# Kernel tuning notes

Hardware: AMD Instinct MI355X
Metric: run time of the kernel (lower is better)

## Reference

```python
import jax, jax.numpy as jnp
import numpy as np

D_MODEL = 1024
N_HEADS = 16
D_HEAD = 64


def setup_inputs() -> dict:
    key = jax.random.key(0)
    ks = jax.random.split(key, 9)
    B, T = 2, 2048
    s_in = 1.0 / np.sqrt(D_MODEL)
    s_o = 1.0 / np.sqrt(N_HEADS * D_HEAD)
    return {
        "x": jax.random.normal(ks[0], (B, T, D_MODEL), dtype=jnp.float32),
        "wq": jax.random.normal(ks[1], (D_MODEL, N_HEADS * D_HEAD), dtype=jnp.float32) * s_in,
        "bq": jax.random.normal(ks[2], (N_HEADS * D_HEAD,), dtype=jnp.float32) * 0.01,
        "wk": jax.random.normal(ks[3], (D_MODEL, N_HEADS * D_HEAD), dtype=jnp.float32) * s_in,
        "bk": jax.random.normal(ks[4], (N_HEADS * D_HEAD,), dtype=jnp.float32) * 0.01,
        "wv": jax.random.normal(ks[5], (D_MODEL, N_HEADS * D_HEAD), dtype=jnp.float32) * s_in,
        "bv": jax.random.normal(ks[6], (N_HEADS * D_HEAD,), dtype=jnp.float32) * 0.01,
        "wo": jax.random.normal(ks[7], (N_HEADS * D_HEAD, D_MODEL), dtype=jnp.float32) * s_o,
        "bo": jax.random.normal(ks[8], (D_MODEL,), dtype=jnp.float32) * 0.01,
    }


def reference(x, wq, bq, wk, bk, wv, bv, wo, bo):
    B, T, _ = x.shape
    H, Dh = N_HEADS, D_HEAD
    # projections -> [B, H, T, Dh]
    q = (x @ wq + bq).reshape(B, T, H, Dh).transpose(0, 2, 1, 3)
    k = (x @ wk + bk).reshape(B, T, H, Dh).transpose(0, 2, 1, 3)
    v = (x @ wv + bv).reshape(B, T, H, Dh).transpose(0, 2, 1, 3)
    scale = 1.0 / np.sqrt(Dh).astype(np.float32)
    attn = jnp.einsum("bhqd,bhkd->bhqk", q, k) * scale  # [B,H,T,T]
    causal = jnp.tril(jnp.ones((T, T), dtype=bool))
    attn = jnp.where(causal, attn, jnp.float32(-jnp.inf))
    attn = jax.nn.softmax(attn, axis=-1)
    out = jnp.einsum("bhqk,bhkd->bhqd", attn, v)  # [B,H,T,Dh]
    out = out.transpose(0, 2, 1, 3).reshape(B, T, H * Dh)
    return out @ wo + bo
```

## Files before the change

kernel.cpp:

```cpp
#include <hip/hip_runtime.h>
#include <math.h>

#define D_MODEL 1024
#define N_HEADS 16
#define D_HEAD  64
#define B_SZ    2
#define T_SEQ   2048
#define WN_ELEMS (1024u * 1024u)

typedef short bf16x8 __attribute__((ext_vector_type(8)));
typedef short bf16x4 __attribute__((ext_vector_type(4)));
typedef float f32x4  __attribute__((ext_vector_type(4)));
typedef unsigned short us4 __attribute__((ext_vector_type(4)));

__device__ __forceinline__ unsigned short f2bf(float f) {
  union { float f; unsigned u; } v; v.f = f;
  unsigned r = v.u + 0x7FFFu + ((v.u >> 16) & 1u);
  return (unsigned short)(r >> 16);
}
__device__ __forceinline__ float bf2f(unsigned short s) {
  union { unsigned u; float f; } v; v.u = ((unsigned)s) << 16;
  return v.f;
}
__device__ __forceinline__ unsigned pack2_rtz(float lo, float hi) {
  union { float f; unsigned u; } a, b; a.f = hi; b.f = lo;
  return __builtin_amdgcn_perm(a.u, b.u, 0x07060302u);
}

__device__ __forceinline__ void async_copy16(const unsigned short* g, unsigned short* l) {
  __builtin_amdgcn_global_load_lds(
      (__attribute__((address_space(1))) void*)(g),
      (__attribute__((address_space(3))) void*)(l), 16, 0, 0);
}


__device__ __forceinline__ unsigned short* opart_ptr(
    unsigned short* wtd, unsigned short* xbd, int p) {
  const size_t off = (size_t)p * 2048;
  const size_t RA  = (size_t)3 * 1024 * 1024;
  return (off < RA) ? (wtd + off) : (xbd + (off - RA));
}

__global__ __launch_bounds__(256) void conv_all(
    const float* __restrict__ x,
    const float* __restrict__ wq, const float* __restrict__ wk,
    const float* __restrict__ wv, const float* __restrict__ wo,
    unsigned short* __restrict__ wt, unsigned short* __restrict__ xb)
{
  const int z = blockIdx.z;
  if (z < 4) {
    const float* W = (z == 0) ? wq : (z == 1) ? wk : (z == 2) ? wv : wo;
    unsigned short* O = wt + (size_t)z * WN_ELEMS;
    __shared__ float t[32][33];
    const int tx = threadIdx.x & 31, ty = threadIdx.x >> 5;
    const int kb = blockIdx.x * 32, nb = blockIdx.y * 32;
    #pragma unroll
    for (int i = 0; i < 4; i++)
      t[ty + i * 8][tx] = W[(size_t)(kb + ty + i * 8) * D_MODEL + nb + tx];
    __syncthreads();
    const int tid = threadIdx.x;
    const int mi  = tid >> 7;
    const int f   = (tid & 127) * 4;
    const int qd  = f >> 7;
    const int lrr = (f >> 3) & 15;
    const int e0  = f & 7;
    const int kt  = kb >> 6, hf = (kb >> 5) & 1, fbn = nb >> 5;
    us4 o;
    #pragma unroll
    for (int j = 0; j < 4; j++)
      o[j] = f2bf(t[qd * 8 + e0 + j][mi * 16 + lrr]);
    *(us4*)&O[((size_t)(fbn * 16 + kt) * 4 + (mi * 2 + hf)) * 512 + f] = o;
  } else {
    const int row = (z - 4) * 1024 + blockIdx.y * 32 + (threadIdx.x >> 3);
    const int col = blockIdx.x * 32 + (threadIdx.x & 7) * 4;
    float4 v = *(const float4*)&x[(size_t)row * D_MODEL + col];
    us4 o = { f2bf(v.x), f2bf(v.y), f2bf(v.z), f2bf(v.w) };
    *(us4*)&xb[(size_t)row * D_MODEL + col] = o;
  }
}

#define BKg 64
#define NTg (D_MODEL / BKg)
#define QSCALE 0.180336879f

__global__ __launch_bounds__(256) void qkv_gemm(
    const unsigned short* __restrict__ A, const unsigned short* __restrict__ Bt,
    const float* __restrict__ bq, const float* __restrict__ bk,
    const float* __restrict__ bv, unsigned short* __restrict__ qkv,
    unsigned short* __restrict__ vT)
{
  __shared__ unsigned short As[2][128 * BKg];

  const int tid  = threadIdx.x;
  const int wv   = tid >> 6;
  const int lane = tid & 63;
  const int lr   = lane & 15;
  const int quad = lane >> 4;
  const int wm   = wv >> 1;
  const int wn   = wv & 1;
  const int row0 = blockIdx.x * 128;
  const int col0 = blockIdx.y * 64;
  const int K = D_MODEL;

  const int mid = col0 >> 10;
  const float* bias = (mid == 0) ? bq : (mid == 1) ? bk : bv;

  f32x4 acc[8];
  #pragma unroll
  for (int i = 0; i < 8; i++) acc[i] = (f32x4){0.f, 0.f, 0.f, 0.f};

  auto stageA = [&](int buf, int k0) {
    #pragma unroll
    for (int it = 0; it < 4; it++) {
      const int gg = wv * 256 + it * 64 + lane;
      const int r  = gg >> 3;
      const int gc = ((gg & 7) ^ (r & 7)) * 8;
      async_copy16(A + (size_t)(row0 + r) * K + k0 + gc,
                   &As[buf][(size_t)(wv * 256 + it * 64) * 8]);
    }
  };

  const int wsel = (mid == 2) ? wn : wm;
  const int fb   = ((col0 & 1023) >> 5) + wsel;
  const unsigned short* Wp =
      Bt + (size_t)mid * WN_ELEMS + (size_t)fb * (16 * 2048) + lane * 8;

  auto loadW = [&](int kt, bf16x8 (&W)[2][2]) {
    #pragma unroll
    for (int mi = 0; mi < 2; mi++)
      #pragma unroll
      for (int hf = 0; hf < 2; hf++)
        W[mi][hf] = *(const bf16x8*)&Wp[((size_t)kt * 4 + mi * 2 + hf) * 512];
  };

  const int xrow = (mid == 2) ? wm : wn;

  bf16x8 Wc[2][2], Wn[2][2];
  loadW(0, Wc);
  stageA(0, 0);
  int cur = 0;

  auto kstep = [&](int t, bf16x8 (&Wuse)[2][2], bf16x8 (&Wpre)[2][2]) {
    __syncthreads();

    bf16x8 xF[4][2];
    #pragma unroll
    for (int hf = 0; hf < 2; hf++) {
      const int kc = ((hf * 4 + quad) ^ (lr & 7)) * 8;
      #pragma unroll
      for (int ni = 0; ni < 4; ni++)
        xF[ni][hf] = *(const bf16x8*)&As[cur][(xrow * 64 + ni * 16 + lr) * BKg + kc];
    }

    if (t + 1 < NTg) {
      stageA(cur ^ 1, (t + 1) * BKg);
      loadW(t + 1, Wpre);
    }

    if (mid == 2) {
      #pragma unroll
      for (int hf = 0; hf < 2; hf++)
        #pragma unroll
        for (int mi = 0; mi < 4; mi++)
          #pragma unroll
          for (int ni = 0; ni < 2; ni++)
            acc[mi * 2 + ni] = __builtin_amdgcn_mfma_f32_16x16x32_bf16(
                xF[mi][hf], Wuse[ni][hf], acc[mi * 2 + ni], 0, 0, 0);
    } else {
      #pragma unroll
      for (int hf = 0; hf < 2; hf++)
        #pragma unroll
        for (int mi = 0; mi < 2; mi++)
          #pragma unroll
          for (int ni = 0; ni < 4; ni++)
            acc[mi * 4 + ni] = __builtin_amdgcn_mfma_f32_16x16x32_bf16(
                Wuse[mi][hf], xF[ni][hf], acc[mi * 4 + ni], 0, 0, 0);
    }
    cur ^= 1;
  };

  #pragma unroll 1
  for (int t = 0; t < NTg; t += 2) {
    kstep(t,     Wc, Wn);
    kstep(t + 1, Wn, Wc);
  }

  if (mid == 2) {
    #pragma unroll
    for (int ni = 0; ni < 2; ni++) {
      const int nn = (col0 & 1023) + wn * 32 + ni * 16 + lr;
      const float bv_ = bias[nn];
      const int h = nn >> 6, d = nn & 63;
      #pragma unroll
      for (int mi = 0; mi < 4; mi++) {
        const int t0_ = row0 + wm * 64 + mi * 16 + quad * 4;
        const int b = t0_ >> 11, tl = t0_ & 2047;
        us4 o;
        #pragma unroll
        for (int i = 0; i < 4; i++) o[i] = f2bf(acc[mi * 2 + ni][i] + bv_);
        *(us4*)&vT[((size_t)(b * N_HEADS + h) * D_HEAD + d) * T_SEQ + tl] = o;
      }
    }
  } else {
    unsigned short* dst = qkv + (size_t)mid * (4096u * 1024u);
    const float qs = (mid == 0) ? QSCALE : 1.0f;
    #pragma unroll
    for (int ni = 0; ni < 4; ni++) {
      const int t = row0 + wn * 64 + ni * 16 + lr;
      const int b = t >> 11, tl = t & 2047;
      #pragma unroll
      for (int mi = 0; mi < 2; mi++) {
        const int f = (col0 & 1023) + wm * 32 + mi * 16 + quad * 4;
        const int h = f >> 6, d = f & 63;
        const float4 b4 = *(const float4*)&bias[f];
        us4 o;
        o[0] = f2bf((acc[mi * 4 + ni][0] + b4.x) * qs);
        o[1] = f2bf((acc[mi * 4 + ni][1] + b4.y) * qs);
        o[2] = f2bf((acc[mi * 4 + ni][2] + b4.z) * qs);
        o[3] = f2bf((acc[mi * 4 + ni][3] + b4.w) * qs);
        *(us4*)&dst[((size_t)(b * N_HEADS + h) * T_SEQ + tl) * D_HEAD + d] = o;
      }
    }
  }
}

__global__ __launch_bounds__(256) void mfma_gemm(
    const unsigned short* __restrict__ A, const unsigned short* __restrict__ Bt,
    const float* __restrict__ bias, float* __restrict__ C,
    int M, int N, int K)
{
  __shared__ unsigned short As[2][128 * BKg];

  const int tid  = threadIdx.x;
  const int wv   = tid >> 6;
  const int lane = tid & 63;
  const int lr   = lane & 15;
  const int quad = lane >> 4;
  const int wm   = wv >> 1;
  const int wn   = wv & 1;
  const int row0 = blockIdx.x * 128;
  const int col0 = blockIdx.y * 64;

  f32x4 acc[4][2];
  #pragma unroll
  for (int mi = 0; mi < 4; mi++)
    #pragma unroll
    for (int ni = 0; ni < 2; ni++) acc[mi][ni] = (f32x4){0.f, 0.f, 0.f, 0.f};

  auto stageA = [&](int buf, int k0) {
    #pragma unroll
    for (int it = 0; it < 4; it++) {
      const int gg = wv * 256 + it * 64 + lane;
      const int r  = gg >> 3;
      const int gc = ((gg & 7) ^ (r & 7)) * 8;
      async_copy16(A + (size_t)(row0 + r) * K + k0 + gc,
                   &As[buf][(size_t)(wv * 256 + it * 64) * 8]);
    }
  };

  const int fb = (col0 >> 5) + wn;
  const unsigned short* Wp = Bt + (size_t)fb * (16 * 2048) + lane * 8;
  auto loadW = [&](int kt, bf16x8 (&W)[2][2]) {
    #pragma unroll
    for (int ni = 0; ni < 2; ni++)
      #pragma unroll
      for (int hf = 0; hf < 2; hf++)
        W[ni][hf] = *(const bf16x8*)&Wp[((size_t)kt * 4 + ni * 2 + hf) * 512];
  };

  const int NT = K / BKg;
  bf16x8 Wc[2][2], Wn[2][2];
  loadW(0, Wc);
  stageA(0, 0);
  int cur = 0;

  auto kstep = [&](int t, bf16x8 (&Wuse)[2][2], bf16x8 (&Wpre)[2][2]) {
    __syncthreads();

    bf16x8 aF[4][2];
    #pragma unroll
    for (int hf = 0; hf < 2; hf++) {
      const int kc = ((hf * 4 + quad) ^ (lr & 7)) * 8;
      #pragma unroll
      for (int mi = 0; mi < 4; mi++)
        aF[mi][hf] = *(const bf16x8*)&As[cur][(wm * 64 + mi * 16 + lr) * BKg + kc];
    }

    if (t + 1 < NT) {
      stageA(cur ^ 1, (t + 1) * BKg);
      loadW(t + 1, Wpre);
    }

    #pragma unroll
    for (int hf = 0; hf < 2; hf++)
      #pragma unroll
      for (int mi = 0; mi < 4; mi++)
        #pragma unroll
        for (int ni = 0; ni < 2; ni++)
          acc[mi][ni] = __builtin_amdgcn_mfma_f32_16x16x32_bf16(
              aF[mi][hf], Wuse[ni][hf], acc[mi][ni], 0, 0, 0);
    cur ^= 1;
  };

  #pragma unroll 1
  for (int t = 0; t < NT; t += 2) {
    kstep(t,     Wc, Wn);
    kstep(t + 1, Wn, Wc);
  }

  #pragma unroll
  for (int ni = 0; ni < 2; ni++) {
    const int n = col0 + wn * 32 + ni * 16 + lr;
    const float bv = bias[n];
    #pragma unroll
    for (int mi = 0; mi < 4; mi++) {
      #pragma unroll
      for (int i = 0; i < 4; i++) {
        const int m = row0 + wm * 64 + mi * 16 + quad * 4 + i;
        C[(size_t)m * N + n] = acc[mi][ni][i] + bv;
      }
    }
  }
}

__global__ __launch_bounds__(256) void flash_part(
    const unsigned short* __restrict__ Q, const unsigned short* __restrict__ K,
    const unsigned short* __restrict__ Vt, unsigned short* __restrict__ Out,
    unsigned short* __restrict__ OpA, unsigned short* __restrict__ OpB,
    float* __restrict__ Lpart)
{
  const int bh = blockIdx.x;
  const int y  = blockIdx.y;
  int g, md;
  if (y < 28) { g = 15 - (y >> 1); md = 1 + (y & 1); }
  else        { g = 29 - y; md = 0; }

  const int b  = bh >> 4;
  const int h  = bh & 15;

  const unsigned short* Qb = Q  + (size_t)bh * T_SEQ * D_HEAD;
  const unsigned short* Kb = K  + (size_t)bh * T_SEQ * D_HEAD;
  const unsigned short* Vb = Vt + (size_t)bh * D_HEAD * T_SEQ;

  __shared__ __align__(16) unsigned short Ks[2][64 * 64];
  __shared__ __align__(16) unsigned short Vs[2][64 * 64];

  const int tid  = threadIdx.x;
  const int wv4  = tid >> 6;
  const int lane = tid & 63;
  const int lr   = lane & 15;
  const int quad = lane >> 4;

  const int qg      = 4 * g + wv4;
  const int q0      = qg * 32;
  const int my_full = 2 * g + 1 + (wv4 >> 1);
  const int tstart  = (md == 2) ? (g + 1) : 0;
  const int bend    = (md == 1) ? (g + 1) : (2 * g + 2);
  const int my_end  = (md == 1) ? (g + 1) : my_full;

  const int cbase = (tid & ~63);
  const int rr = tid >> 3;
  const int gcf = ((tid & 7) ^ (rr & 7)) * 8;
  const unsigned short* kp0 = Kb + (size_t)rr * D_HEAD + gcf;
  const unsigned short* vp0 = Vb + (size_t)rr * T_SEQ + gcf;

  auto stage = [&](int buf, int tile) {
    const unsigned short* kt = kp0 + (size_t)tile * (64 * D_HEAD);
    const unsigned short* vt = vp0 + (size_t)tile * 64;
    async_copy16(kt,                    &Ks[buf][(size_t)cbase * 8]);
    async_copy16(kt + 32 * D_HEAD,      &Ks[buf][(size_t)(256 + cbase) * 8]);
    async_copy16(vt,                    &Vs[buf][(size_t)cbase * 8]);
    async_copy16(vt + (size_t)32 * T_SEQ, &Vs[buf][(size_t)(256 + cbase) * 8]);
  };

  bf16x8 bQ[2][2];
  #pragma unroll
  for (int qb = 0; qb < 2; qb++)
    #pragma unroll
    for (int kh = 0; kh < 2; kh++)
      bQ[qb][kh] = *(const bf16x8*)&Qb[(size_t)(q0 + qb * 16 + lr) * D_HEAD + kh * 32 + quad * 8];

  f32x4 oacc[2][4];
  #pragma unroll
  for (int qb = 0; qb < 2; qb++)
    #pragma unroll
    for (int dt = 0; dt < 4; dt++) oacc[qb][dt] = (f32x4){0.f, 0.f, 0.f, 0.f};
  f32x4 lacc[2] = {(f32x4){0.f, 0.f, 0.f, 0.f}, (f32x4){0.f, 0.f, 0.f, 0.f}};

  const bf16x4 vONE = {(short)0x3F80, (short)0x3F80, (short)0x3F80, (short)0x3F80};

  int cur = 0;
  stage(0, tstart);

  for (int j = tstart; j < bend; j++) {
    __syncthreads();
    const bool act = (j < my_end);
    const unsigned short* KsB = &Ks[cur][0];
    const unsigned short* VsB = &Vs[cur][0];
    const int kv0 = j * 64;

    bf16x8 aK[4][2];
    bf16x4 aV[4][4];
    if (act) {
      #pragma unroll
      for (int nt = 0; nt < 4; nt++) {
        const int row = nt * 16 + lr;
        #pragma unroll
        for (int kh = 0; kh < 2; kh++) {
          const int sc = (kh * 4 + quad) ^ (row & 7);
          aK[nt][kh] = *(const bf16x8*)&KsB[row * 64 + sc * 8];
        }
      }
      #pragma unroll
      for (int dt = 0; dt < 4; dt++) {
        const int row = dt * 16 + lr;
        #pragma unroll
        for (int ks = 0; ks < 4; ks++) {
          const int sc = (ks * 2 + (quad >> 1)) ^ (row & 7);
          aV[dt][ks] = *(const bf16x4*)&VsB[row * 64 + sc * 8 + (quad & 1) * 4];
        }
      }
    }

    if (j + 1 < bend) stage(cur ^ 1, j + 1);

    if (act) {
      f32x4 sacc[2][4];
      __builtin_amdgcn_s_setprio(1);
      #pragma unroll
      for (int nt = 0; nt < 4; nt++) {
        #pragma unroll
        for (int qb = 0; qb < 2; qb++) {
          f32x4 c = (f32x4){0.f, 0.f, 0.f, 0.f};
          c = __builtin_amdgcn_mfma_f32_16x16x32_bf16(aK[nt][0], bQ[qb][0], c, 0, 0, 0);
          c = __builtin_amdgcn_mfma_f32_16x16x32_bf16(aK[nt][1], bQ[qb][1], c, 0, 0, 0);
          sacc[qb][nt] = c;
        }
      }
      __builtin_amdgcn_s_setprio(0);

      const bool diag = (j == my_full - 1);
      bf16x4 bP[2][4];
      #pragma unroll
      for (int qb = 0; qb < 2; qb++) {
        if (diag) {
          const int qcol = q0 + qb * 16 + lr;
          #pragma unroll
          for (int nt = 0; nt < 4; nt++)
            #pragma unroll
            for (int i = 0; i < 4; i++)
              if (kv0 + nt * 16 + quad * 4 + i > qcol) sacc[qb][nt][i] = -INFINITY;
        }
        #pragma unroll
        for (int nt = 0; nt < 4; nt++) {
          float p[4];
          #pragma unroll
          for (int i = 0; i < 4; i++)
            p[i] = __builtin_amdgcn_exp2f(sacc[qb][nt][i]);
          union { unsigned u[2]; bf16x4 v; } pk;
          pk.u[0] = pack2_rtz(p[0], p[1]);
          pk.u[1] = pack2_rtz(p[2], p[3]);
          bP[qb][nt] = pk.v;
        }
      }

      __builtin_amdgcn_s_setprio(1);
      #pragma unroll
      for (int ks = 0; ks < 4; ks++) {
        #pragma unroll
        for (int qb = 0; qb < 2; qb++) {
          lacc[qb] = __builtin_amdgcn_mfma_f32_16x16x16bf16_1k(
              vONE, bP[qb][ks], lacc[qb], 0, 0, 0);
          #pragma unroll
          for (int dt = 0; dt < 4; dt++)
            oacc[qb][dt] = __builtin_amdgcn_mfma_f32_16x16x16bf16_1k(
                aV[dt][ks], bP[qb][ks], oacc[qb][dt], 0, 0, 0);
        }
      }
      __builtin_amdgcn_s_setprio(0);
    }
    cur ^= 1;
  }

  float l_i[2] = {lacc[0][0], lacc[1][0]};

  if (md == 0) {
    #pragma unroll
    for (int qb = 0; qb < 2; qb++) {
      const float invl = __builtin_amdgcn_rcpf(l_i[qb]);
      const size_t orow = (size_t)(b * T_SEQ + q0 + qb * 16 + lr) * D_MODEL + h * D_HEAD;
      #pragma unroll
      for (int dt = 0; dt < 4; dt++) {
        us4 o;
        #pragma unroll
        for (int i = 0; i < 4; i++) o[i] = f2bf(oacc[qb][dt][i] * invl);
        *(us4*)&Out[orow + dt * 16 + quad * 4] = o;
      }
    }
  } else {
    const int s = md - 1;
    const int p = (bh * 56 + (qg - 8)) * 2 + s;
    unsigned short* Op = opart_ptr(OpA, OpB, p);
    if (quad == 0) {
      Lpart[(p * 2 + 0) * 16 + lr] = l_i[0];
      Lpart[(p * 2 + 1) * 16 + lr] = l_i[1];
    }
    #pragma unroll
    for (int qb = 0; qb < 2; qb++) {
      #pragma unroll
      for (int dt = 0; dt < 4; dt++) {
        us4 o;
        #pragma unroll
        for (int i = 0; i < 4; i++) o[i] = f2bf(oacc[qb][dt][i]);
        *(us4*)&Op[(size_t)(((qb * 4 + dt) * 64) + lane) * 4] = o;
      }
    }
  }
}

__global__ __launch_bounds__(64) void flash_reduce(
    unsigned short* __restrict__ OpA, unsigned short* __restrict__ OpB,
    const float* __restrict__ Lpart, unsigned short* __restrict__ Out)
{
  const int bh  = blockIdx.x;
  const int qgr = blockIdx.y;
  const int q0  = (8 + qgr) * 32;
  const int b   = bh >> 4;
  const int h   = bh & 15;
  const int lane = threadIdx.x;
  const int lr   = lane & 15;
  const int quad = lane >> 4;

  const int item = bh * 56 + qgr;
  const int p0 = item * 2, p1 = item * 2 + 1;
  const unsigned short* O0 = opart_ptr(OpA, OpB, p0);
  const unsigned short* O1 = opart_ptr(OpA, OpB, p1);

  #pragma unroll
  for (int qb = 0; qb < 2; qb++) {
    const float l0 = Lpart[(p0 * 2 + qb) * 16 + lr];
    const float l1 = Lpart[(p1 * 2 + qb) * 16 + lr];
    const float invL = __builtin_amdgcn_rcpf(l0 + l1);
    const size_t orow = (size_t)(b * T_SEQ + q0 + qb * 16 + lr) * D_MODEL + h * D_HEAD;
    #pragma unroll
    for (int dt = 0; dt < 4; dt++) {
      us4 o0 = *(const us4*)&O0[(size_t)(((qb * 4 + dt) * 64) + lane) * 4];
      us4 o1 = *(const us4*)&O1[(size_t)(((qb * 4 + dt) * 64) + lane) * 4];
      us4 o;
      #pragma unroll
      for (int i = 0; i < 4; i++)
        o[i] = f2bf((bf2f(o0[i]) + bf2f(o1[i])) * invL);
      *(us4*)&Out[orow + dt * 16 + quad * 4] = o;
    }
  }
}

extern "C" void kernel_launch(void* const* d_in, const int* in_sizes, int n_in,
                              void* d_out, int out_size, void* d_ws, size_t ws_size,
                              hipStream_t stream) {
  (void)in_sizes; (void)n_in; (void)out_size; (void)ws_size;

  const float* x  = (const float*)d_in[0];
  const float* wq = (const float*)d_in[1];
  const float* bq = (const float*)d_in[2];
  const float* wk = (const float*)d_in[3];
  const float* bk = (const float*)d_in[4];
  const float* wv = (const float*)d_in[5];
  const float* bv = (const float*)d_in[6];
  const float* wo = (const float*)d_in[7];
  const float* bo = (const float*)d_in[8];
  float* out = (float*)d_out;

  const int M = B_SZ * T_SEQ;
  const int N = D_MODEL;
  const int K = D_MODEL;
  const size_t MN = (size_t)M * N;
  const size_t WN = (size_t)N * N;

  unsigned short* wt    = (unsigned short*)d_ws;
  unsigned short* xb    = wt + 4 * WN;
  unsigned short* qkv   = xb + MN;
  unsigned short* qb    = qkv;
  unsigned short* kb    = qkv + MN;
  unsigned short* vT    = qkv + 2 * MN;
  unsigned short* attnb = vT + MN;
  float* Lpart = (float*)(attnb + MN);

  conv_all<<<dim3(32, 32, 8), dim3(256), 0, stream>>>(x, wq, wk, wv, wo, wt, xb);

  qkv_gemm<<<dim3(M / 128, 48), dim3(256), 0, stream>>>(xb, wt, bq, bk, bv, qkv, vT);

  flash_part<<<dim3(B_SZ * N_HEADS, 30), dim3(256), 0, stream>>>(
      qb, kb, vT, attnb, wt, xb, Lpart);
  flash_reduce<<<dim3(B_SZ * N_HEADS, 56), dim3(64), 0, stream>>>(
      wt, xb, Lpart, attnb);

  mfma_gemm<<<dim3(M / 128, N / 64), dim3(256), 0, stream>>>(attnb, wt + 3 * WN, bo, out, M, N, K);
}
```

Baseline: 184.7 us.

## Triple-buffer QKV GEMM loads with prefetch distance two and explicit vmcnt waits

Converts the QKV projection GEMM from double to triple buffering. Both the A tile in LDS and the W fragments in registers are now prefetched two k-steps ahead, and the loop is fully unrolled. Explicit s_waitcnt vmcnt plus an s_barrier replace the plain __syncthreads, so loads stay in flight across iterations. This is meant to hide global-memory latency better, at the cost of 50% more LDS and extra W registers, which may reduce occupancy.

```diff
diff --git a/kernel.cpp b/kernel.cpp
--- a/kernel.cpp
+++ b/kernel.cpp
@@ -89,7 +89,7 @@
     const float* __restrict__ bv, unsigned short* __restrict__ qkv,
     unsigned short* __restrict__ vT)
 {
-  __shared__ unsigned short As[2][128 * BKg];
+  __shared__ unsigned short As[3][128 * BKg];
 
   const int tid  = threadIdx.x;
   const int wv   = tid >> 6;
@@ -125,23 +125,28 @@
   const unsigned short* Wp =
       Bt + (size_t)mid * WN_ELEMS + (size_t)fb * (16 * 2048) + lane * 8;
 
-  auto loadW = [&](int kt, bf16x8 (&W)[2][2]) {
+  bf16x8 Wb[3][2][2];
+  auto loadW = [&](int kt, int bank) {
     #pragma unroll
     for (int mi = 0; mi < 2; mi++)
       #pragma unroll
       for (int hf = 0; hf < 2; hf++)
-        W[mi][hf] = *(const bf16x8*)&Wp[((size_t)kt * 4 + mi * 2 + hf) * 512];
+        Wb[bank][mi][hf] = *(const bf16x8*)&Wp[((size_t)kt * 4 + mi * 2 + hf) * 512];
   };
 
   const int xrow = (mid == 2) ? wm : wn;
 
-  bf16x8 Wc[2][2], Wn[2][2];
-  loadW(0, Wc);
+  loadW(0, 0);
   stageA(0, 0);
-  int cur = 0;
-
-  auto kstep = [&](int t, bf16x8 (&Wuse)[2][2], bf16x8 (&Wpre)[2][2]) {
-    __syncthreads();
+  loadW(1, 1);
+  stageA(1, BKg);
+  asm volatile("s_waitcnt vmcnt(8)" ::: "memory");
+  __builtin_amdgcn_sched_barrier(0);
+  __builtin_amdgcn_s_barrier();
+
+  #pragma unroll
+  for (int t = 0; t < NTg; ++t) {
+    const int cb = t % 3;
 
     bf16x8 xF[4][2];
     #pragma unroll
@@ -149,12 +154,12 @@
       const int kc = ((hf * 4 + quad) ^ (lr & 7)) * 8;
       #pragma unroll
       for (int ni = 0; ni < 4; ni++)
-        xF[ni][hf] = *(const bf16x8*)&As[cur][(xrow * 64 + ni * 16 + lr) * BKg + kc];
-    }
-
-    if (t + 1 < NTg) {
-      stageA(cur ^ 1, (t + 1) * BKg);
-      loadW(t + 1, Wpre);
+        xF[ni][hf] = *(const bf16x8*)&As[cb][(xrow * 64 + ni * 16 + lr) * BKg + kc];
+    }
+
+    if (t + 2 < NTg) {
+      loadW(t + 2, (t + 2) % 3);
+      stageA((t + 2) % 3, (t + 2) * BKg);
     }
 
     if (mid == 2) {
@@ -165,7 +170,7 @@
           #pragma unroll
           for (int ni = 0; ni < 2; ni++)
             acc[mi * 2 + ni] = __builtin_amdgcn_mfma_f32_16x16x32_bf16(
-                xF[mi][hf], Wuse[ni][hf], acc[mi * 2 + ni], 0, 0, 0);
+                xF[mi][hf], Wb[cb][ni][hf], acc[mi * 2 + ni], 0, 0, 0);
     } else {
       #pragma unroll
       for (int hf = 0; hf < 2; hf++)
@@ -174,15 +179,18 @@
           #pragma unroll
           for (int ni = 0; ni < 4; ni++)
             acc[mi * 4 + ni] = __builtin_amdgcn_mfma_f32_16x16x32_bf16(
-                Wuse[mi][hf], xF[ni][hf], acc[mi * 4 + ni], 0, 0, 0);
-    }
-    cur ^= 1;
-  };
-
-  #pragma unroll 1
-  for (int t = 0; t < NTg; t += 2) {
-    kstep(t,     Wc, Wn);
-    kstep(t + 1, Wn, Wc);
+                Wb[cb][mi][hf], xF[ni][hf], acc[mi * 4 + ni], 0, 0, 0);
+    }
+
+    if (t + 1 < NTg) {
+      if (t + 2 < NTg) {
+        asm volatile("s_waitcnt vmcnt(8)" ::: "memory");
+      } else {
+        asm volatile("s_waitcnt vmcnt(0)" ::: "memory");
+      }
+      __builtin_amdgcn_sched_barrier(0);
+      __builtin_amdgcn_s_barrier();
+    }
   }
 
   if (mid == 2) {
```

New measurement: 190.8 us. 1.03x slower.
